# Optimization experiments

Measured on AMD Instinct MI355X. Metric: run time of the kernel, lower is better.

The kernel has to match this reference:

```python
import jax, jax.numpy as jnp
import numpy as np


def setup_inputs() -> dict:
    key = jax.random.key(0)
    k1, k2, k3, k4, k5, k6 = jax.random.split(key, 6)
    B, HID, SP, H, W = 256, 1024, 2048, 14, 14
    hidden = jax.random.normal(k1, (B, HID), dtype=jnp.float32)
    spatial_features = jax.random.normal(k2, (B, SP, H, W), dtype=jnp.float32)
    # attention MLP params: Linear(hid+sp -> hid), Tanh, Linear(hid -> 1)
    s1 = 1.0 / np.sqrt(HID + SP)
    W1 = jax.random.uniform(k3, (HID + SP, HID), dtype=jnp.float32, minval=-s1, maxval=s1)
    b1 = jax.random.uniform(k4, (HID,), dtype=jnp.float32, minval=-s1, maxval=s1)
    s2 = 1.0 / np.sqrt(HID)
    W2 = jax.random.uniform(k5, (HID, 1), dtype=jnp.float32, minval=-s2, maxval=s2)
    b2 = jax.random.uniform(k6, (1,), dtype=jnp.float32, minval=-s2, maxval=s2)
    return {"hidden": hidden, "spatial_features": spatial_features,
            "W1": W1, "b1": b1, "W2": W2, "b2": b2}


def reference(hidden, spatial_features, W1, b1, W2, b2):
    B, C, H, W = spatial_features.shape
    # [B, H*W, C]
    sp = spatial_features.reshape(B, C, H * W).transpose(0, 2, 1)
    hid = hidden[:, None, :]  # [B, 1, HID]
    # Split the concat-matmul: [hid|sp] @ W1 == hid @ W1_h + sp @ W1_s
    HID = hidden.shape[1]
    W1h, W1s = W1[:HID], W1[HID:]
    pre = jnp.einsum('bh,hd->bd', hidden, W1h)[:, None, :] \
        + jnp.einsum('bnc,cd->bnd', sp, W1s) + b1  # [B, HW, HID]
    scores = jnp.einsum('bnd,d->bn', jnp.tanh(pre), W2[:, 0]) + b2[0]  # [B, HW]
    attn = jax.nn.softmax(scores, axis=1)
    context = jnp.einsum('bn,bnc->bc', attn, sp)  # [B, C]
    return context, attn
```

## Files before the change

### kernel.cpp

```cpp
#include <hip/hip_runtime.h>
#include <hip/hip_bf16.h>
#include <hip/hip_fp16.h>
#include <math.h>

#define B_   256
#define HID_ 1024
#define SP_  2048
#define N_   196
#define NJ_  (B_ * N_)
#define SPB_ (SP_ * N_)

typedef float    f32x4 __attribute__((ext_vector_type(4)));
typedef _Float16 f16x8 __attribute__((ext_vector_type(8)));

#define GLOBAL_AS(p) ((const __attribute__((address_space(1))) void*)(p))
#define LDS_AS(p)    ((__attribute__((address_space(3))) void*)(p))

__device__ __forceinline__ float fast_tanh(float x) {
    const float e = exp2f(x * 2.8853900817779268f);
    return 1.f - 2.f / (e + 1.f);
}

__global__ __launch_bounds__(256) void k1_h1(
    const float* __restrict__ hidden, const float* __restrict__ W1,
    const float* __restrict__ b1, float* __restrict__ h1)
{
    __shared__ float hs[4][HID_];
    const int t = threadIdx.x;
    const int d = blockIdx.x * 256 + t;
    const int b0 = blockIdx.y * 4;

    for (int i = t; i < 4 * HID_; i += 256)
        hs[i >> 10][i & 1023] = hidden[(size_t)(b0 + (i >> 10)) * HID_ + (i & 1023)];
    __syncthreads();

    float acc[4] = {};
    for (int h = 0; h < HID_; ++h) {
        const float w = W1[(size_t)h * HID_ + d];
#pragma unroll
        for (int i = 0; i < 4; ++i) acc[i] += hs[i][h] * w;
    }
    const float bias = b1[d];
#pragma unroll
    for (int i = 0; i < 4; ++i)
        h1[(size_t)(b0 + i) * HID_ + d] = acc[i] + bias;
}

__global__ __launch_bounds__(256) void k0a_packA(
    const float* __restrict__ W1, __half* __restrict__ Ah)
{
    const size_t idx = (size_t)blockIdx.x * 256 + threadIdx.x;
    const int c8 = idx & 7;
    const int dd = (idx >> 3) & 127;
    const int cg = (idx >> 10) & 3;
    const int ks = (idx >> 12) & 63;
    const int dt = idx >> 18;
    const int d = dt * 128 + dd;
    const int c = ks * 32 + cg * 8 + c8;
    Ah[idx] = __float2half(W1[(size_t)(HID_ + c) * HID_ + d]);
}

__global__ __launch_bounds__(256) void k0b_packB(
    const float* __restrict__ spatial, __half* __restrict__ Bh)
{
    const int jt2 = blockIdx.x;
    const int ks  = blockIdx.y;
    const int jj  = threadIdx.x;

    const int j = jt2 * 256 + jj;
    const int b = j / N_;
    const int n = j - b * N_;
    const float* spj = spatial + (size_t)b * SPB_ + n;
    __half* outb = Bh + (((size_t)jt2 * 64 + ks) * 4) * 2048 + jj * 8;

#pragma unroll
    for (int cg = 0; cg < 4; ++cg) {
        const float* src = spj + (size_t)(ks * 32 + cg * 8) * N_;
        f16x8 v;
#pragma unroll
        for (int c8 = 0; c8 < 8; ++c8)
            v[c8] = (_Float16)src[(size_t)c8 * N_];
        *(f16x8*)(outb + (size_t)cg * 2048) = v;
    }
}

__global__ __launch_bounds__(256, 2) void k2_pipe(
    const __half* __restrict__ Ah, const __half* __restrict__ Bh,
    const float* __restrict__ W2, const float* __restrict__ h1,
    float* __restrict__ ps)
{
    extern __shared__ __align__(16) short ldsb[];

    const int tid = threadIdx.x;
    const int l  = tid & 63;
    const int w  = tid >> 6;
    const int wm = w >> 1;
    const int wn = w & 1;
    const int cg = l >> 4;
    const int rr = l & 15;

    const int orig = blockIdx.x;
    const int wgid = (orig & 7) * 196 + (orig >> 3);
    const int jt2 = wgid >> 3;
    const int dt  = wgid & 7;

    const __half* apack = Ah + ((size_t)dt * 64) * 4096;
    const __half* bpack = Bh + ((size_t)jt2 * 64) * 8192;

    f32x4 acc[4][8] = {};

#define STAGE_A(KT, SLOT) do {                                                  \
        const __half* as_ = apack + (size_t)(KT) * 4096;                        \
        short* ad_ = ldsb + (SLOT) * 12288 + w * 1024;                          \
        __builtin_amdgcn_global_load_lds(GLOBAL_AS(as_ + w * 1024 + l * 8),     \
                                         LDS_AS(ad_), 16, 0, 0);                \
        __builtin_amdgcn_global_load_lds(GLOBAL_AS(as_ + w * 1024 + 512 + l * 8),\
                                         LDS_AS(ad_ + 512), 16, 0, 0);          \
    } while (0)

#define STAGE_B(KT, SLOT) do {                                                  \
        const __half* bs_ = bpack + (size_t)(KT) * 8192;                        \
        short* bd_ = ldsb + (SLOT) * 12288 + 4096 + w * 2048;                   \
        _Pragma("unroll")                                                       \
        for (int i_ = 0; i_ < 4; ++i_)                                          \
            __builtin_amdgcn_global_load_lds(                                   \
                GLOBAL_AS(bs_ + w * 2048 + i_ * 512 + l * 8),                   \
                LDS_AS(bd_ + i_ * 512), 16, 0, 0);                              \
    } while (0)

#define STEP(KT, CSLOT, SSLOT, DO_STAGE, VMC) do {                              \
        const short* ab_ = ldsb + (CSLOT) * 12288;                              \
        const short* bb_ = ab_ + 4096;                                          \
        f16x8 af[2], bf[8], af2[2];                                             \
        _Pragma("unroll")                                                       \
        for (int ni = 0; ni < 8; ++ni)                                          \
            bf[ni] = *(const f16x8*)&bb_[(cg * 256 + wn * 128 + ni * 16 + rr) * 8];\
        _Pragma("unroll")                                                       \
        for (int mi = 0; mi < 2; ++mi)                                          \
            af[mi] = *(const f16x8*)&ab_[(cg * 128 + wm * 64 + mi * 16 + rr) * 8];\
        if (DO_STAGE) STAGE_A((KT) + 2, SSLOT);                                 \
        __builtin_amdgcn_s_barrier();                                           \
        asm volatile("s_waitcnt lgkmcnt(0)" ::: "memory");                      \
        __builtin_amdgcn_sched_barrier(0);                                      \
        __builtin_amdgcn_s_setprio(1);                                          \
        _Pragma("unroll")                                                       \
        for (int mi = 0; mi < 2; ++mi)                                          \
            _Pragma("unroll")                                                   \
            for (int ni = 0; ni < 8; ++ni)                                      \
                acc[mi][ni] = __builtin_amdgcn_mfma_f32_16x16x32_f16(           \
                    af[mi], bf[ni], acc[mi][ni], 0, 0, 0);                      \
        __builtin_amdgcn_s_setprio(0);                                          \
        _Pragma("unroll")                                                       \
        for (int mi = 0; mi < 2; ++mi)                                          \
            af2[mi] = *(const f16x8*)&ab_[(cg * 128 + wm * 64 + (mi + 2) * 16 + rr) * 8];\
        if (DO_STAGE) STAGE_B((KT) + 2, SSLOT);                                 \
        asm volatile("s_waitcnt vmcnt(" #VMC ")" ::: "memory");                 \
        __builtin_amdgcn_s_barrier();                                           \
        asm volatile("s_waitcnt lgkmcnt(0)" ::: "memory");                      \
        __builtin_amdgcn_sched_barrier(0);                                      \
        __builtin_amdgcn_s_setprio(1);                                          \
        _Pragma("unroll")                                                       \
        for (int mi = 0; mi < 2; ++mi)                                          \
            _Pragma("unroll")                                                   \
            for (int ni = 0; ni < 8; ++ni)                                      \
                acc[mi + 2][ni] = __builtin_amdgcn_mfma_f32_16x16x32_f16(       \
                    af2[mi], bf[ni], acc[mi + 2][ni], 0, 0, 0);                 \
        __builtin_amdgcn_s_setprio(0);                                          \
    } while (0)

    STAGE_A(0, 0); STAGE_B(0, 0);
    STAGE_A(1, 1); STAGE_B(1, 1);
    asm volatile("s_waitcnt vmcnt(6)" ::: "memory");
    __builtin_amdgcn_s_barrier();

#pragma unroll 1
    for (int kt = 0; kt < 60; kt += 3) {
        STEP(kt + 0, 0, 2, true, 6);
        STEP(kt + 1, 1, 0, true, 6);
        STEP(kt + 2, 2, 1, true, 6);
    }
    STEP(60, 0, 2, true, 6);
    STEP(61, 1, 0, true, 6);
    STEP(62, 2, 0, false, 0);
    STEP(63, 0, 0, false, 0);

#undef STAGE_A
#undef STAGE_B
#undef STEP

    const int dbase = dt * 128 + wm * 64;
    float w2v[4][4];
#pragma unroll
    for (int mi = 0; mi < 4; ++mi)
#pragma unroll
        for (int q = 0; q < 4; ++q)
            w2v[mi][q] = W2[dbase + mi * 16 + cg * 4 + q];

    float partial[8];
#pragma unroll
    for (int ni = 0; ni < 8; ++ni) {
        const int j = jt2 * 256 + wn * 128 + ni * 16 + rr;
        const int bj = j / N_;
        const float* h1p = h1 + (size_t)bj * HID_ + dbase;
        float s = 0.f;
#pragma unroll
        for (int mi = 0; mi < 4; ++mi)
#pragma unroll
            for (int q = 0; q < 4; ++q)
                s += fast_tanh(acc[mi][ni][q] + h1p[mi * 16 + cg * 4 + q]) * w2v[mi][q];
        partial[ni] = s;
    }

    float* red = (float*)ldsb;
    __syncthreads();
    red[tid] = 0.f;
    __syncthreads();
#pragma unroll
    for (int ni = 0; ni < 8; ++ni)
        atomicAdd(&red[wn * 128 + ni * 16 + rr], partial[ni]);
    __syncthreads();
    ps[(size_t)dt * NJ_ + (size_t)jt2 * 256 + tid] = red[tid];
}

__global__ __launch_bounds__(256) void k2_fb(
    const float* __restrict__ spatial, const float* __restrict__ W1,
    const float* __restrict__ W2, const float* __restrict__ h1,
    float* __restrict__ ps)
{
    __shared__ float As[32][64];
    __shared__ float Bs[32][64];
    const int t = threadIdx.x;
    const int d0 = blockIdx.x * 64;
    const int j0 = blockIdx.y * 64;
    const int ld = t & 63, lk = t >> 6;
    const float* Aptr = W1 + (size_t)(HID_ + lk) * HID_ + (d0 + ld);
    const int j = j0 + ld;
    const int bb = j / N_, nn = j - bb * N_;
    const float* Bptr = spatial + (size_t)bb * SPB_ + (size_t)lk * N_ + nn;
    const int tr = t >> 4, tc = t & 15;
    float acc[4][4] = {};
    for (int c0 = 0; c0 < SP_; c0 += 32) {
#pragma unroll
        for (int i = 0; i < 8; ++i) {
            As[lk + 4 * i][ld] = Aptr[(size_t)(c0 + 4 * i) * HID_];
            Bs[lk + 4 * i][ld] = Bptr[(size_t)(c0 + 4 * i) * N_];
        }
        __syncthreads();
#pragma unroll
        for (int k = 0; k < 32; ++k) {
            float av[4], bv[4];
            *(float4*)av = *(const float4*)&As[k][tr * 4];
            *(float4*)bv = *(const float4*)&Bs[k][tc * 4];
#pragma unroll
            for (int di = 0; di < 4; ++di)
#pragma unroll
                for (int ji = 0; ji < 4; ++ji)
                    acc[di][ji] += av[di] * bv[ji];
        }
        __syncthreads();
    }
    float w2v[4];
#pragma unroll
    for (int di = 0; di < 4; ++di) w2v[di] = W2[d0 + tr * 4 + di];
    float partial[4] = {};
#pragma unroll
    for (int ji = 0; ji < 4; ++ji) {
        const int jg = j0 + tc * 4 + ji;
        const int bj = jg / N_;
        const float* h1row = h1 + (size_t)bj * HID_ + d0 + tr * 4;
#pragma unroll
        for (int di = 0; di < 4; ++di)
            partial[ji] += tanhf(acc[di][ji] + h1row[di]) * w2v[di];
    }
    __shared__ float red[64];
    if (t < 64) red[t] = 0.f;
    __syncthreads();
#pragma unroll
    for (int ji = 0; ji < 4; ++ji)
        atomicAdd(&red[tc * 4 + ji], partial[ji]);
    __syncthreads();
    if (t < 64)
        ps[(size_t)blockIdx.x * NJ_ + j0 + t] = red[t];
}

__global__ __launch_bounds__(256) void k3_softmax(
    const float* __restrict__ ps, float* __restrict__ attn, int nslices)
{
    const int b = blockIdx.x;
    const int t = threadIdx.x;
    __shared__ float sdata[256];

    float s = -1e30f;
    if (t < N_) {
        s = 0.f;
        for (int dt = 0; dt < nslices; ++dt)
            s += ps[(size_t)dt * NJ_ + b * N_ + t];
    }
    sdata[t] = s;
    __syncthreads();
    for (int off = 128; off > 0; off >>= 1) {
        if (t < off) sdata[t] = fmaxf(sdata[t], sdata[t + off]);
        __syncthreads();
    }
    const float m = sdata[0];
    __syncthreads();
    const float e = (t < N_) ? expf(s - m) : 0.f;
    sdata[t] = e;
    __syncthreads();
    for (int off = 128; off > 0; off >>= 1) {
        if (t < off) sdata[t] += sdata[t + off];
        __syncthreads();
    }
    const float inv = 1.f / sdata[0];
    if (t < N_) attn[(size_t)b * N_ + t] = e * inv;
}

__global__ __launch_bounds__(256) void k4_ctx_bh(
    const __half* __restrict__ Bh, const float* __restrict__ attn,
    float* __restrict__ ctx)
{
    const int wid  = blockIdx.x * 4 + (threadIdx.x >> 6);
    const int lane = threadIdx.x & 63;
    const int b  = wid >> 8;
    const int sub = wid & 255;
    const int ks = sub >> 2;
    const int cg = sub & 3;

    const float* at = attn + (size_t)b * N_;
    const int jbase = b * N_;

    float p[8] = {};
#pragma unroll
    for (int it = 0; it < 4; ++it) {
        const int n = it * 64 + lane;
        if (n < N_) {
            const int j = jbase + n;
            const int jt2 = j >> 8;
            const int jj  = j & 255;
            const f16x8 v = *(const f16x8*)(Bh +
                ((((size_t)jt2 * 64 + ks) * 4 + cg) * 2048) + jj * 8);
            const float a = at[n];
#pragma unroll
            for (int q = 0; q < 8; ++q)
                p[q] += a * (float)v[q];
        }
    }
#pragma unroll
    for (int off = 32; off > 0; off >>= 1)
#pragma unroll
        for (int q = 0; q < 8; ++q)
            p[q] += __shfl_down(p[q], off, 64);

    if (lane == 0) {
        float* out = ctx + (size_t)b * 2048 + ks * 32 + cg * 8;
#pragma unroll
        for (int q = 0; q < 8; ++q) out[q] = p[q];
    }
}

__global__ __launch_bounds__(256) void k4_context(
    const float* __restrict__ spatial, const float* __restrict__ attn,
    float* __restrict__ ctx)
{
    const int wid = (blockIdx.x * 256 + threadIdx.x) >> 6;
    const int lane = threadIdx.x & 63;
    const int b = wid >> 11;
    const int c = wid & 2047;
    const float* sp = spatial + (size_t)b * SPB_ + (size_t)c * N_;
    const float* at = attn + (size_t)b * N_;

    float sum = 0.f;
    if (lane < 49) {
        const float4 s4 = ((const float4*)sp)[lane];
        const float4 a4 = ((const float4*)at)[lane];
        sum = s4.x * a4.x + s4.y * a4.y + s4.z * a4.z + s4.w * a4.w;
    }
#pragma unroll
    for (int off = 32; off > 0; off >>= 1)
        sum += __shfl_down(sum, off, 64);
    if (lane == 0)
        ctx[(size_t)b * 2048 + c] = sum;
}

extern "C" void kernel_launch(void* const* d_in, const int* in_sizes, int n_in,
                              void* d_out, int out_size, void* d_ws, size_t ws_size,
                              hipStream_t stream)
{
    const float* hidden  = (const float*)d_in[0];
    const float* spatial = (const float*)d_in[1];
    const float* W1      = (const float*)d_in[2];
    const float* b1      = (const float*)d_in[3];
    const float* W2      = (const float*)d_in[4];

    float* out_ctx  = (float*)d_out;
    float* out_attn = (float*)d_out + (size_t)B_ * 2048;

    char* ws = (char*)d_ws;
    float* h1 = (float*)ws;
    float* psb = (float*)(ws + (1u << 20));

    const size_t offAh = 8u << 20;
    const size_t offBh = 16u << 20;
    const size_t szB   = (size_t)196 * 64 * 8192 * 2;
    const size_t needed = offBh + szB;

    k1_h1<<<dim3(4, 64), 256, 0, stream>>>(hidden, W1, b1, h1);

    if (ws_size >= needed) {
        __half* Ah = (__half*)(ws + offAh);
        __half* Bh = (__half*)(ws + offBh);
        k0a_packA<<<dim3(8192), 256, 0, stream>>>(W1, Ah);
        k0b_packB<<<dim3(196, 64), 256, 0, stream>>>(spatial, Bh);
        (void)hipFuncSetAttribute((const void*)k2_pipe,
                                  hipFuncAttributeMaxDynamicSharedMemorySize,
                                  73728);
        k2_pipe<<<dim3(1568), 256, 73728, stream>>>(Ah, Bh, W2, h1, psb);
        k3_softmax<<<dim3(B_), 256, 0, stream>>>(psb, out_attn, 8);
        k4_ctx_bh<<<dim3(16384), 256, 0, stream>>>(Bh, out_attn, out_ctx);
    } else {
        k2_fb<<<dim3(16, 784), 256, 0, stream>>>(spatial, W1, W2, h1, psb);
        k3_softmax<<<dim3(B_), 256, 0, stream>>>(psb, out_attn, 16);
        k4_context<<<dim3((B_ * 2048) / 4), 256, 0, stream>>>(spatial, out_attn, out_ctx);
    }
}
```

Before: 453.7 us.

## Split hidden projection over K with reduction; vectorize spatial pack loads

The hidden-state projection is split into four K-chunks launched as a third grid dimension, with partial sums written to workspace and a separate reduce kernel that adds them and the bias. This quadruples block count for a GEMV-like kernel that previously had only 256 blocks, at the cost of an extra launch and partial-buffer traffic. The spatial pack kernel now has each thread read float4 runs of four consecutive positions instead of scalar strided loads, so global reads are wider and better coalesced. Both changes apply only on the large-workspace path.

```diff
diff --git a/kernel.cpp b/kernel.cpp
--- a/kernel.cpp
+++ b/kernel.cpp
@@ -19,6 +19,44 @@
 __device__ __forceinline__ float fast_tanh(float x) {
     const float e = exp2f(x * 2.8853900817779268f);
     return 1.f - 2.f / (e + 1.f);
+}
+
+__global__ __launch_bounds__(256) void k1_h1p(
+    const float* __restrict__ hidden, const float* __restrict__ W1,
+    float* __restrict__ h1p)
+{
+    __shared__ float hs[4][256];
+    const int t  = threadIdx.x;
+    const int d  = blockIdx.x * 256 + t;
+    const int b0 = blockIdx.y * 4;
+    const int h0 = blockIdx.z * 256;
+
+    for (int i = t; i < 4 * 256; i += 256)
+        hs[i >> 8][i & 255] = hidden[(size_t)(b0 + (i >> 8)) * HID_ + h0 + (i & 255)];
+    __syncthreads();
+
+    float acc[4] = {};
+    for (int h = 0; h < 256; ++h) {
+        const float w = W1[(size_t)(h0 + h) * HID_ + d];
+#pragma unroll
+        for (int i = 0; i < 4; ++i) acc[i] += hs[i][h] * w;
+    }
+#pragma unroll
+    for (int i = 0; i < 4; ++i)
+        h1p[((size_t)blockIdx.z * B_ + b0 + i) * HID_ + d] = acc[i];
+}
+
+__global__ __launch_bounds__(256) void k1_reduce(
+    const float* __restrict__ h1p, const float* __restrict__ b1,
+    float* __restrict__ h1)
+{
+    const size_t idx = (size_t)blockIdx.x * 256 + threadIdx.x;
+    const int d = idx & (HID_ - 1);
+    float s = b1[d];
+#pragma unroll
+    for (int hq = 0; hq < 4; ++hq)
+        s += h1p[(size_t)hq * B_ * HID_ + idx];
+    h1[idx] = s;
 }
 
 __global__ __launch_bounds__(256) void k1_h1(
@@ -65,23 +103,29 @@
 {
     const int jt2 = blockIdx.x;
     const int ks  = blockIdx.y;
-    const int jj  = threadIdx.x;
-
-    const int j = jt2 * 256 + jj;
-    const int b = j / N_;
-    const int n = j - b * N_;
-    const float* spj = spatial + (size_t)b * SPB_ + n;
-    __half* outb = Bh + (((size_t)jt2 * 64 + ks) * 4) * 2048 + jj * 8;
-
-#pragma unroll
-    for (int cg = 0; cg < 4; ++cg) {
-        const float* src = spj + (size_t)(ks * 32 + cg * 8) * N_;
-        f16x8 v;
-#pragma unroll
-        for (int c8 = 0; c8 < 8; ++c8)
-            v[c8] = (_Float16)src[(size_t)c8 * N_];
-        *(f16x8*)(outb + (size_t)cg * 2048) = v;
-    }
+    const int t   = threadIdx.x;
+    const int cg  = t >> 6;
+    const int jg  = t & 63;
+
+    const int j0 = jt2 * 256 + jg * 4;
+    const int b  = j0 / N_;
+    const int n0 = j0 - b * N_;
+    const float* src = spatial + (size_t)b * SPB_
+                     + (size_t)(ks * 32 + cg * 8) * N_ + n0;
+
+    f16x8 v[4];
+#pragma unroll
+    for (int c8 = 0; c8 < 8; ++c8) {
+        const float4 f = *(const float4*)(src + (size_t)c8 * N_);
+        v[0][c8] = (_Float16)f.x;
+        v[1][c8] = (_Float16)f.y;
+        v[2][c8] = (_Float16)f.z;
+        v[3][c8] = (_Float16)f.w;
+    }
+    __half* outb = Bh + (((size_t)jt2 * 64 + ks) * 4 + cg) * 2048 + jg * 32;
+#pragma unroll
+    for (int q = 0; q < 4; ++q)
+        *(f16x8*)(outb + q * 8) = v[q];
 }
 
 __global__ __launch_bounds__(256, 2) void k2_pipe(
@@ -396,19 +440,20 @@
     float* out_attn = (float*)d_out + (size_t)B_ * 2048;
 
     char* ws = (char*)d_ws;
-    float* h1 = (float*)ws;
+    float* h1  = (float*)ws;
     float* psb = (float*)(ws + (1u << 20));
+    float* h1p = (float*)(ws + (4u << 20));
 
     const size_t offAh = 8u << 20;
     const size_t offBh = 16u << 20;
     const size_t szB   = (size_t)196 * 64 * 8192 * 2;
     const size_t needed = offBh + szB;
 
-    k1_h1<<<dim3(4, 64), 256, 0, stream>>>(hidden, W1, b1, h1);
-
     if (ws_size >= needed) {
         __half* Ah = (__half*)(ws + offAh);
         __half* Bh = (__half*)(ws + offBh);
+        k1_h1p<<<dim3(4, 64, 4), 256, 0, stream>>>(hidden, W1, h1p);
+        k1_reduce<<<dim3(1024), 256, 0, stream>>>(h1p, b1, h1);
         k0a_packA<<<dim3(8192), 256, 0, stream>>>(W1, Ah);
         k0b_packB<<<dim3(196, 64), 256, 0, stream>>>(spatial, Bh);
         (void)hipFuncSetAttribute((const void*)k2_pipe,
@@ -418,6 +463,7 @@
         k3_softmax<<<dim3(B_), 256, 0, stream>>>(psb, out_attn, 8);
         k4_ctx_bh<<<dim3(16384), 256, 0, stream>>>(Bh, out_attn, out_ctx);
     } else {
+        k1_h1<<<dim3(4, 64), 256, 0, stream>>>(hidden, W1, b1, h1);
         k2_fb<<<dim3(16, 784), 256, 0, stream>>>(spatial, W1, W2, h1, psb);
         k3_softmax<<<dim3(B_), 256, 0, stream>>>(psb, out_attn, 16);
         k4_context<<<dim3((B_ * 2048) / 4), 256, 0, stream>>>(spatial, out_attn, out_ctx);
```

Measured after the change: 416.6 us. 1.09x faster.
